# Kernel optimization log

Hardware: AMD Instinct MI355X
Metric: run time of the kernel (lower is better)

The kernel has to match this reference:

```python
import jax, jax.numpy as jnp
import numpy as np

NEG_SLOPE = 0.2  # PyG GATConv default leaky_relu slope


def gat_conv(x, src, dst, W, a_src, a_dst, b, num_nodes):
    """One PyG-style GATConv layer (concat over heads).
    x: [N, F_in]; src/dst: [E] (message flows src -> dst);
    W: [F_in, H*C]; a_src/a_dst: [H, C]; b: [H*C].
    """
    H, C = a_src.shape
    h = (x @ W).reshape(num_nodes, H, C)              # [N, H, C]
    alpha_src = jnp.sum(h * a_src, axis=-1)           # [N, H]
    alpha_dst = jnp.sum(h * a_dst, axis=-1)           # [N, H]
    e = jax.nn.leaky_relu(alpha_src[src] + alpha_dst[dst], NEG_SLOPE)  # [E, H]
    # segment softmax over incoming edges of each destination node
    m = jax.ops.segment_max(e, dst, num_segments=num_nodes)            # [N, H]
    ex = jnp.exp(e - m[dst])
    s = jax.ops.segment_sum(ex, dst, num_segments=num_nodes)           # [N, H]
    alpha = ex / (s[dst] + 1e-16)                                      # [E, H]
    msg = h[src] * alpha[:, :, None]                                   # [E, H, C]
    out = jax.ops.segment_sum(msg, dst, num_segments=num_nodes)        # [N, H, C]
    return out.reshape(num_nodes, H * C) + b


def setup_inputs() -> dict:
    key = jax.random.key(0)
    ks = jax.random.split(key, 12)
    N, E, F_in, C, H = 50000, 800000, 256, 64, 8
    x = jax.random.normal(ks[0], (N, F_in), dtype=jnp.float32)
    edge_index = jax.random.randint(ks[1], (2, E), 0, N, dtype=jnp.int64)
    glorot = lambda k, shape: jax.random.normal(k, shape, jnp.float32) * np.sqrt(2.0 / (shape[0] + shape[-1]))
    return {
        "x": x,
        "edge_index": edge_index,
        "W1": glorot(ks[2], (F_in, H * C)),
        "att_src1": glorot(ks[3], (H, C)),
        "att_dst1": glorot(ks[4], (H, C)),
        "b1": jnp.zeros((H * C,), jnp.float32),
        "W2": glorot(ks[5], (H * C, 1 * C)),
        "att_src2": glorot(ks[6], (1, C)),
        "att_dst2": glorot(ks[7], (1, C)),
        "b2": jnp.zeros((C,), jnp.float32),
    }


def reference(x, edge_index, W1, att_src1, att_dst1, b1, W2, att_src2, att_dst2, b2):
    N = x.shape[0]
    # add self-loops (PyG GATConv default add_self_loops=True)
    loops = jnp.arange(N, dtype=edge_index.dtype)
    src = jnp.concatenate([edge_index[0], loops])
    dst = jnp.concatenate([edge_index[1], loops])
    h = gat_conv(x, src, dst, W1, att_src1, att_dst1, b1, N)   # [N, 512]
    h = jax.nn.relu(h)                                         # dropout p=0 -> identity
    out = gat_conv(h, src, dst, W2, att_src2, att_dst2, b2, N) # [N, 64]
    return out
```

## Files before the change

### kernel.cpp

```cpp
#include <hip/hip_runtime.h>
#include <hip/hip_bf16.h>
#include <math.h>
#include <type_traits>

#define NEG_SLOPE 0.2f
#define CAP 64

typedef float f32x4 __attribute__((ext_vector_type(4)));
typedef short s16x8 __attribute__((ext_vector_type(8)));
typedef short s16x4 __attribute__((ext_vector_type(4)));

__device__ __forceinline__ float bf2f(ushort s) {
    union { unsigned u; float f; } cv; cv.u = ((unsigned)s) << 16;
    return cv.f;
}
__device__ __forceinline__ ushort f2bf(float f) {
    __hip_bfloat16 b = __float2bfloat16(f);
    union { __hip_bfloat16 b; ushort u; } cv; cv.b = b;
    return cv.u;
}

__device__ __forceinline__ int edge_val(const int* e, long long i, int is64) {
    return is64 ? e[(size_t)(2 * i)] : e[(size_t)i];
}

__global__ void prep_all(const int* __restrict__ e, int* __restrict__ flag,
                         int* __restrict__ counts, int* __restrict__ csr, int N,
                         const float* __restrict__ W1, ushort* __restrict__ W1t, int K1, int N1,
                         const float* __restrict__ W2, ushort* __restrict__ W2t, int K2, int N2) {
    int b = blockIdx.x, tid = threadIdx.x;
    int nbN = (N + 255) >> 8;
    int nbW1 = (K1 * N1 + 255) >> 8;
    if (b < nbN) {
        int i = b * 256 + tid;
        if (i < N) {
            counts[i] = 1;
            csr[(size_t)i * CAP] = i;
        }
    } else if (b == nbN) {
        if (tid < 64) {
            int v = e[2 * tid + 1];
            unsigned long long bl = __ballot(v != 0);
            if (tid == 0) *flag = (bl == 0ull) ? 1 : 0;
        }
    } else if (b < nbN + 1 + nbW1) {
        int idx = (b - nbN - 1) * 256 + tid;
        if (idx < K1 * N1) {
            int k = idx & (K1 - 1), n = idx / K1;
            W1t[(size_t)n * K1 + k] = f2bf(W1[(size_t)k * N1 + n]);
        }
    } else {
        int idx = (b - nbN - 1 - nbW1) * 256 + tid;
        if (idx < K2 * N2) {
            int k = idx & (K2 - 1), n = idx / K2;
            W2t[(size_t)n * K2 + k] = f2bf(W2[(size_t)k * N2 + n]);
        }
    }
}

__global__ void scatter_edges(const int* __restrict__ ebuf, int E,
                              int* __restrict__ counts, int* __restrict__ csr,
                              const int* __restrict__ flag) {
    int i = blockIdx.x * blockDim.x + threadIdx.x;
    if (i >= E) return;
    int is64 = *flag;
    int s = edge_val(ebuf, i, is64);
    int d = edge_val(ebuf, (long long)E + i, is64);
    int pos = atomicAdd(&counts[d], 1);
    if (pos < CAP) csr[(size_t)d * CAP + pos] = s;
}

template <typename AT, typename CT, int BM, int BN, int WR, int WC, int H>
__global__ __launch_bounds__(256) void gemm_mfma(const AT* __restrict__ A,
                                                 const ushort* __restrict__ Bt,
                                                 CT* __restrict__ C,
                                                 const float* __restrict__ att_s,
                                                 const float* __restrict__ att_d,
                                                 float* __restrict__ as_,
                                                 float* __restrict__ ad_,
                                                 int M, int N, int K) {
    constexpr int BK = 64;
    constexpr int MT = BM / WR / 16;
    constexpr int NT = 4;
    static_assert(WR * WC == 4 && BN == WC * 64, "4 waves, 64 cols each");
    __shared__ __align__(16) ushort As[BM][BK + 8];
    __shared__ __align__(16) ushort Bs[BN][BK + 8];

    int tid = threadIdx.x;
    int wid = tid >> 6, lane = tid & 63;
    int wr = wid / WC, wc = wid % WC;
    int bm = blockIdx.y * BM, bn = blockIdx.x * BN;
    int l15 = lane & 15, l4 = lane >> 4;

    f32x4 acc[MT][NT] = {};

    for (int k0 = 0; k0 < K; k0 += BK) {
        if constexpr (std::is_same_v<AT, float>) {
#pragma unroll
            for (int p = 0; p < BM * BK / 1024; ++p) {
                int idx = p * 256 + tid;
                int r = idx >> 4;
                int kc = (idx & 15) << 2;
                float4 v = make_float4(0.f, 0.f, 0.f, 0.f);
                if (bm + r < M) v = *(const float4*)&A[(size_t)(bm + r) * K + k0 + kc];
                ushort* dst = &As[r][kc];
                dst[0] = f2bf(v.x); dst[1] = f2bf(v.y);
                dst[2] = f2bf(v.z); dst[3] = f2bf(v.w);
            }
        } else {
#pragma unroll
            for (int p = 0; p < BM * BK / 2048; ++p) {
                int idx = p * 256 + tid;
                int r = idx >> 3;
                int kc = (idx & 7) << 3;
                s16x8 v = {};
                if (bm + r < M) v = *(const s16x8*)&A[(size_t)(bm + r) * K + k0 + kc];
                *(s16x8*)&As[r][kc] = v;
            }
        }
#pragma unroll
        for (int p = 0; p < BN * BK / 2048; ++p) {
            int idx = p * 256 + tid;
            int n = idx >> 3;
            int kc = (idx & 7) << 3;
            s16x8 v = *(const s16x8*)&Bt[(size_t)(bn + n) * K + k0 + kc];
            *(s16x8*)&Bs[n][kc] = v;
        }
        __syncthreads();
#pragma unroll
        for (int kk = 0; kk < BK; kk += 32) {
            s16x8 af[MT], bf[NT];
            int kb = kk + (l4 << 3);
#pragma unroll
            for (int mt = 0; mt < MT; ++mt)
                af[mt] = *(const s16x8*)&As[wr * (BM / WR) + mt * 16 + l15][kb];
#pragma unroll
            for (int nt = 0; nt < NT; ++nt)
                bf[nt] = *(const s16x8*)&Bs[wc * 64 + nt * 16 + l15][kb];
#pragma unroll
            for (int mt = 0; mt < MT; ++mt)
#pragma unroll
                for (int nt = 0; nt < NT; ++nt)
                    acc[mt][nt] = __builtin_amdgcn_mfma_f32_16x16x32_bf16(af[mt], bf[nt], acc[mt][nt], 0, 0, 0);
        }
        __syncthreads();
    }

    int head = (bn >> 6) + wc;
    float asv[NT], adv[NT];
#pragma unroll
    for (int nt = 0; nt < NT; ++nt) {
        asv[nt] = att_s[head * 64 + nt * 16 + l15];
        adv[nt] = att_d[head * 64 + nt * 16 + l15];
    }
#pragma unroll
    for (int mt = 0; mt < MT; ++mt) {
#pragma unroll
        for (int j = 0; j < 4; ++j) {
            int r = bm + wr * (BM / WR) + mt * 16 + (l4 << 2) + j;
            float ps = 0.f, pd = 0.f;
#pragma unroll
            for (int nt = 0; nt < NT; ++nt) {
                float v = acc[mt][nt][j];
                ps += v * asv[nt];
                pd += v * adv[nt];
            }
#pragma unroll
            for (int off = 1; off < 16; off <<= 1) {
                ps += __shfl_xor(ps, off);
                pd += __shfl_xor(pd, off);
            }
            if (r < M) {
                if (l15 == 0) {
                    as_[(size_t)r * H + head] = ps;
                    ad_[(size_t)r * H + head] = pd;
                }
#pragma unroll
                for (int nt = 0; nt < NT; ++nt) {
                    size_t ci = (size_t)r * N + bn + wc * 64 + nt * 16 + l15;
                    if constexpr (std::is_same_v<CT, float>) C[ci] = acc[mt][nt][j];
                    else C[ci] = f2bf(acc[mt][nt][j]);
                }
            }
        }
    }
}

__global__ __launch_bounds__(256) void gat_fused_l1(
        const ushort* __restrict__ h, const float* __restrict__ as_,
        const float* __restrict__ ad_, const int* __restrict__ counts,
        const int* __restrict__ csr, const float* __restrict__ bias,
        ushort* __restrict__ out1, int N) {
    int n = (blockIdx.x * 256 + threadIdx.x) >> 6;
    if (n >= N) return;
    int l = threadIdx.x & 63;
    size_t base = (size_t)n * CAP;
    int deg = counts[n]; deg = deg > CAP ? CAP : deg;

    int hh = l & 7, e0 = l >> 3;
    float adw = ad_[n * 8 + hh];
    float m = -1e30f, s = 0.f;
    for (int k = e0; k < deg; k += 8) {
        int src = csr[base + k];
        float e = as_[src * 8 + hh] + adw;
        e = e > 0.f ? e : NEG_SLOPE * e;
        float mn = fmaxf(m, e);
        s = s * __expf(m - mn) + __expf(e - mn);
        m = mn;
    }
#pragma unroll
    for (int off = 8; off < 64; off <<= 1) {
        float mo = __shfl_xor(m, off), so = __shfl_xor(s, off);
        float mn = fmaxf(m, mo);
        s = s * __expf(m - mn) + so * __expf(mo - mn);
        m = mn;
    }
    float inv = 1.f / (s + 1e-16f);
    int hd = l >> 3;
    float mh   = __shfl(m, hd);
    float invh = __shfl(inv, hd);
    float adh  = __shfl(adw, hd);

    float acc[8] = {};
    int k = 0;
    for (; k + 4 <= deg; k += 4) {
        int s0 = csr[base + k],     s1 = csr[base + k + 1];
        int s2 = csr[base + k + 2], s3 = csr[base + k + 3];
        s16x8 v0 = *(const s16x8*)&h[((size_t)s0 << 9) + (l << 3)];
        s16x8 v1 = *(const s16x8*)&h[((size_t)s1 << 9) + (l << 3)];
        s16x8 v2 = *(const s16x8*)&h[((size_t)s2 << 9) + (l << 3)];
        s16x8 v3 = *(const s16x8*)&h[((size_t)s3 << 9) + (l << 3)];
        float e0v = as_[s0 * 8 + hd] + adh;
        float e1v = as_[s1 * 8 + hd] + adh;
        float e2v = as_[s2 * 8 + hd] + adh;
        float e3v = as_[s3 * 8 + hd] + adh;
        e0v = e0v > 0.f ? e0v : NEG_SLOPE * e0v;
        e1v = e1v > 0.f ? e1v : NEG_SLOPE * e1v;
        e2v = e2v > 0.f ? e2v : NEG_SLOPE * e2v;
        e3v = e3v > 0.f ? e3v : NEG_SLOPE * e3v;
        float a0 = __expf(e0v - mh);
        float a1 = __expf(e1v - mh);
        float a2 = __expf(e2v - mh);
        float a3 = __expf(e3v - mh);
#pragma unroll
        for (int j = 0; j < 8; ++j)
            acc[j] += a0 * bf2f((ushort)v0[j]) + a1 * bf2f((ushort)v1[j])
                    + a2 * bf2f((ushort)v2[j]) + a3 * bf2f((ushort)v3[j]);
    }
    for (; k < deg; ++k) {
        int s0 = csr[base + k];
        s16x8 v0 = *(const s16x8*)&h[((size_t)s0 << 9) + (l << 3)];
        float e0v = as_[s0 * 8 + hd] + adh;
        e0v = e0v > 0.f ? e0v : NEG_SLOPE * e0v;
        float a0 = __expf(e0v - mh);
#pragma unroll
        for (int j = 0; j < 8; ++j) acc[j] += a0 * bf2f((ushort)v0[j]);
    }
    float4 b0 = *(const float4*)&bias[l * 8];
    float4 b1 = *(const float4*)&bias[l * 8 + 4];
    s16x8 w;
    w[0] = f2bf(fmaxf(acc[0] * invh + b0.x, 0.f));
    w[1] = f2bf(fmaxf(acc[1] * invh + b0.y, 0.f));
    w[2] = f2bf(fmaxf(acc[2] * invh + b0.z, 0.f));
    w[3] = f2bf(fmaxf(acc[3] * invh + b0.w, 0.f));
    w[4] = f2bf(fmaxf(acc[4] * invh + b1.x, 0.f));
    w[5] = f2bf(fmaxf(acc[5] * invh + b1.y, 0.f));
    w[6] = f2bf(fmaxf(acc[6] * invh + b1.z, 0.f));
    w[7] = f2bf(fmaxf(acc[7] * invh + b1.w, 0.f));
    *(s16x8*)&out1[((size_t)n << 9) + (l << 3)] = w;
}

__global__ __launch_bounds__(256) void gat_fused_l2(
        const ushort* __restrict__ h, const float* __restrict__ as_,
        const float* __restrict__ ad_, const int* __restrict__ counts,
        const int* __restrict__ csr, const float* __restrict__ bias,
        float* __restrict__ out, int N) {
    int n = (blockIdx.x * 256 + threadIdx.x) >> 6;
    if (n >= N) return;
    int l = threadIdx.x & 63;
    size_t base = (size_t)n * CAP;
    int deg = counts[n]; deg = deg > CAP ? CAP : deg;
    float adv = ad_[n];

    float m = -1e30f, s = 0.f;
    for (int k = l; k < deg; k += 64) {
        float e = as_[csr[base + k]] + adv;
        e = e > 0.f ? e : NEG_SLOPE * e;
        float mn = fmaxf(m, e);
        s = s * __expf(m - mn) + __expf(e - mn);
        m = mn;
    }
#pragma unroll
    for (int off = 1; off < 64; off <<= 1) {
        float mo = __shfl_xor(m, off), so = __shfl_xor(s, off);
        float mn = fmaxf(m, mo);
        s = s * __expf(m - mn) + so * __expf(mo - mn);
        m = mn;
    }
    float inv = 1.f / (s + 1e-16f);

    int q = l >> 4, c4 = l & 15;
    float a0 = 0.f, a1 = 0.f, a2 = 0.f, a3 = 0.f;
    int k = q;
    for (; k + 12 < deg; k += 16) {
        int sA = csr[base + k],     sB = csr[base + k + 4];
        int sC = csr[base + k + 8], sD = csr[base + k + 12];
        s16x4 vA = *(const s16x4*)&h[((size_t)sA << 6) + (c4 << 2)];
        s16x4 vB = *(const s16x4*)&h[((size_t)sB << 6) + (c4 << 2)];
        s16x4 vC = *(const s16x4*)&h[((size_t)sC << 6) + (c4 << 2)];
        s16x4 vD = *(const s16x4*)&h[((size_t)sD << 6) + (c4 << 2)];
        float eA = as_[sA] + adv, eB = as_[sB] + adv;
        float eC = as_[sC] + adv, eD = as_[sD] + adv;
        eA = eA > 0.f ? eA : NEG_SLOPE * eA;
        eB = eB > 0.f ? eB : NEG_SLOPE * eB;
        eC = eC > 0.f ? eC : NEG_SLOPE * eC;
        eD = eD > 0.f ? eD : NEG_SLOPE * eD;
        float aA = __expf(eA - m), aB = __expf(eB - m);
        float aC = __expf(eC - m), aD = __expf(eD - m);
        a0 += aA * bf2f((ushort)vA[0]) + aB * bf2f((ushort)vB[0])
            + aC * bf2f((ushort)vC[0]) + aD * bf2f((ushort)vD[0]);
        a1 += aA * bf2f((ushort)vA[1]) + aB * bf2f((ushort)vB[1])
            + aC * bf2f((ushort)vC[1]) + aD * bf2f((ushort)vD[1]);
        a2 += aA * bf2f((ushort)vA[2]) + aB * bf2f((ushort)vB[2])
            + aC * bf2f((ushort)vC[2]) + aD * bf2f((ushort)vD[2]);
        a3 += aA * bf2f((ushort)vA[3]) + aB * bf2f((ushort)vB[3])
            + aC * bf2f((ushort)vC[3]) + aD * bf2f((ushort)vD[3]);
    }
    for (; k < deg; k += 4) {
        int sA = csr[base + k];
        s16x4 vA = *(const s16x4*)&h[((size_t)sA << 6) + (c4 << 2)];
        float eA = as_[sA] + adv;
        eA = eA > 0.f ? eA : NEG_SLOPE * eA;
        float aA = __expf(eA - m);
        a0 += aA * bf2f((ushort)vA[0]);
        a1 += aA * bf2f((ushort)vA[1]);
        a2 += aA * bf2f((ushort)vA[2]);
        a3 += aA * bf2f((ushort)vA[3]);
    }
    a0 += __shfl_xor(a0, 16); a0 += __shfl_xor(a0, 32);
    a1 += __shfl_xor(a1, 16); a1 += __shfl_xor(a1, 32);
    a2 += __shfl_xor(a2, 16); a2 += __shfl_xor(a2, 32);
    a3 += __shfl_xor(a3, 16); a3 += __shfl_xor(a3, 32);
    if (q == 0) {
        float4 bv = *(const float4*)&bias[c4 << 2];
        float4 r;
        r.x = a0 * inv + bv.x; r.y = a1 * inv + bv.y;
        r.z = a2 * inv + bv.z; r.w = a3 * inv + bv.w;
        *(float4*)&out[((size_t)n << 6) + (c4 << 2)] = r;
    }
}

extern "C" void kernel_launch(void* const* d_in, const int* in_sizes, int n_in,
                              void* d_out, int out_size, void* d_ws, size_t ws_size,
                              hipStream_t stream) {
    const float* x    = (const float*)d_in[0];
    const int*   ebuf = (const int*)d_in[1];
    const float* W1   = (const float*)d_in[2];
    const float* aS1  = (const float*)d_in[3];
    const float* aD1  = (const float*)d_in[4];
    const float* b1   = (const float*)d_in[5];
    const float* W2   = (const float*)d_in[6];
    const float* aS2  = (const float*)d_in[7];
    const float* aD2  = (const float*)d_in[8];
    const float* b2   = (const float*)d_in[9];
    float* out = (float*)d_out;

    const int F_in = 256, H1 = 8, HC1 = 512, C2 = 64;
    int N = in_sizes[0] / F_in;
    int E = in_sizes[1] / 2;

    char* ws = (char*)d_ws;
    size_t off = 0;
    auto alloc = [&](size_t bytes) -> void* {
        void* p = ws + off;
        off = (off + bytes + 255) & ~(size_t)255;
        return p;
    };
    ushort* h1b    = (ushort*)alloc((size_t)N * HC1 * 2);
    ushort* out1b  = (ushort*)alloc((size_t)N * HC1 * 2);
    float* as1     = (float*)alloc((size_t)N * H1 * 4);
    float* ad1     = (float*)alloc((size_t)N * H1 * 4);
    float* as2     = (float*)alloc((size_t)N * 4);
    float* ad2     = (float*)alloc((size_t)N * 4);
    int*   counts  = (int*)alloc((size_t)N * 4);
    int*   csr     = (int*)alloc((size_t)N * CAP * 4);
    int*   flag    = (int*)alloc(64);
    ushort* W1t    = (ushort*)alloc((size_t)F_in * HC1 * 2);
    ushort* W2t    = (ushort*)alloc((size_t)HC1 * C2 * 2);
    ushort* h2b    = h1b;

    int nbN = (N + 255) >> 8;
    int nbW1 = (F_in * HC1 + 255) >> 8;
    int nbW2 = (HC1 * C2 + 255) >> 8;

    prep_all<<<nbN + 1 + nbW1 + nbW2, 256, 0, stream>>>(
        ebuf, flag, counts, csr, N, W1, W1t, F_in, HC1, W2, W2t, HC1, C2);
    scatter_edges<<<(E + 255) / 256, 256, 0, stream>>>(ebuf, E, counts, csr, flag);

    {
        dim3 g(HC1 / 128, (N + 127) / 128);
        gemm_mfma<float, ushort, 128, 128, 2, 2, 8><<<g, 256, 0, stream>>>(
            x, W1t, h1b, aS1, aD1, as1, ad1, N, HC1, F_in);
    }
    gat_fused_l1<<<(N + 3) / 4, 256, 0, stream>>>(h1b, as1, ad1, counts, csr, b1, out1b, N);

    {
        dim3 g(1, (N + 63) / 64);
        gemm_mfma<ushort, ushort, 64, 64, 4, 1, 1><<<g, 256, 0, stream>>>(
            out1b, W2t, h2b, aS2, aD2, as2, ad2, N, C2, HC1);
    }
    gat_fused_l2<<<(N + 3) / 4, 256, 0, stream>>>(h2b, as2, ad2, counts, csr, b2, out, N);
}
```

Measured before the change: 306.3 us.

## Merge edge scatter into first GEMM launch with wider 512-thread tiles

The separate scatter_edges kernel is folded into the layer-1 GEMM launch. Leading blocks do the atomic CSR fill, and the remaining blocks run the GEMM, so the two independent pieces of work overlap in one launch. The GEMM core becomes a device function generic over wave count, and layer 1 now uses 128x256 tiles with 8 waves (512 threads). The larger tiles roughly double shared memory per block and raise register pressure, which may lower occupancy.

```diff
diff --git a/kernel.cpp b/kernel.cpp
--- a/kernel.cpp
+++ b/kernel.cpp
@@ -58,38 +58,29 @@
     }
 }
 
-__global__ void scatter_edges(const int* __restrict__ ebuf, int E,
-                              int* __restrict__ counts, int* __restrict__ csr,
-                              const int* __restrict__ flag) {
-    int i = blockIdx.x * blockDim.x + threadIdx.x;
-    if (i >= E) return;
-    int is64 = *flag;
-    int s = edge_val(ebuf, i, is64);
-    int d = edge_val(ebuf, (long long)E + i, is64);
-    int pos = atomicAdd(&counts[d], 1);
-    if (pos < CAP) csr[(size_t)d * CAP + pos] = s;
-}
-
 template <typename AT, typename CT, int BM, int BN, int WR, int WC, int H>
-__global__ __launch_bounds__(256) void gemm_mfma(const AT* __restrict__ A,
-                                                 const ushort* __restrict__ Bt,
-                                                 CT* __restrict__ C,
-                                                 const float* __restrict__ att_s,
-                                                 const float* __restrict__ att_d,
-                                                 float* __restrict__ as_,
-                                                 float* __restrict__ ad_,
-                                                 int M, int N, int K) {
+__device__ __forceinline__ void gemm_core(int bx, int by,
+                                          const AT* __restrict__ A,
+                                          const ushort* __restrict__ Bt,
+                                          CT* __restrict__ C,
+                                          const float* __restrict__ att_s,
+                                          const float* __restrict__ att_d,
+                                          float* __restrict__ as_,
+                                          float* __restrict__ ad_,
+                                          int M, int N, int K) {
     constexpr int BK = 64;
+    constexpr int WAVES = WR * WC;
+    constexpr int THREADS = WAVES * 64;
     constexpr int MT = BM / WR / 16;
     constexpr int NT = 4;
-    static_assert(WR * WC == 4 && BN == WC * 64, "4 waves, 64 cols each");
+    static_assert(BN == WC * 64, "each wave-col owns one 64-col head");
     __shared__ __align__(16) ushort As[BM][BK + 8];
     __shared__ __align__(16) ushort Bs[BN][BK + 8];
 
     int tid = threadIdx.x;
     int wid = tid >> 6, lane = tid & 63;
     int wr = wid / WC, wc = wid % WC;
-    int bm = blockIdx.y * BM, bn = blockIdx.x * BN;
+    int bm = by * BM, bn = bx * BN;
     int l15 = lane & 15, l4 = lane >> 4;
 
     f32x4 acc[MT][NT] = {};
@@ -97,8 +88,8 @@
     for (int k0 = 0; k0 < K; k0 += BK) {
         if constexpr (std::is_same_v<AT, float>) {
 #pragma unroll
-            for (int p = 0; p < BM * BK / 1024; ++p) {
-                int idx = p * 256 + tid;
+            for (int p = 0; p < BM * BK / (4 * THREADS); ++p) {
+                int idx = p * THREADS + tid;
                 int r = idx >> 4;
                 int kc = (idx & 15) << 2;
                 float4 v = make_float4(0.f, 0.f, 0.f, 0.f);
@@ -109,8 +100,8 @@
             }
         } else {
 #pragma unroll
-            for (int p = 0; p < BM * BK / 2048; ++p) {
-                int idx = p * 256 + tid;
+            for (int p = 0; p < BM * BK / (8 * THREADS); ++p) {
+                int idx = p * THREADS + tid;
                 int r = idx >> 3;
                 int kc = (idx & 7) << 3;
                 s16x8 v = {};
@@ -119,8 +110,8 @@
             }
         }
 #pragma unroll
-        for (int p = 0; p < BN * BK / 2048; ++p) {
-            int idx = p * 256 + tid;
+        for (int p = 0; p < BN * BK / (8 * THREADS); ++p) {
+            int idx = p * THREADS + tid;
             int n = idx >> 3;
             int kc = (idx & 7) << 3;
             s16x8 v = *(const s16x8*)&Bt[(size_t)(bn + n) * K + k0 + kc];
@@ -184,6 +175,37 @@
             }
         }
     }
+}
+
+__global__ __launch_bounds__(512) void gemm1_scatter(
+        const int* __restrict__ ebuf, int E, int* __restrict__ counts,
+        int* __restrict__ csr, const int* __restrict__ flag, int nScatter,
+        const float* __restrict__ A, const ushort* __restrict__ Bt,
+        ushort* __restrict__ C, const float* __restrict__ att_s,
+        const float* __restrict__ att_d, float* __restrict__ as_,
+        float* __restrict__ ad_, int M, int N, int K) {
+    if ((int)blockIdx.x < nScatter) {
+        int i = blockIdx.x * 512 + threadIdx.x;
+        if (i >= E) return;
+        int is64 = *flag;
+        int s = edge_val(ebuf, i, is64);
+        int d = edge_val(ebuf, (long long)E + i, is64);
+        int pos = atomicAdd(&counts[d], 1);
+        if (pos < CAP) csr[(size_t)d * CAP + pos] = s;
+        return;
+    }
+    int g = blockIdx.x - nScatter;
+    gemm_core<float, ushort, 128, 256, 2, 4, 8>(g & 1, g >> 1, A, Bt, C,
+                                                att_s, att_d, as_, ad_, M, N, K);
+}
+
+template <typename AT, typename CT, int BM, int BN, int WR, int WC, int H>
+__global__ __launch_bounds__(WR * WC * 64) void gemm_mfma(
+        const AT* __restrict__ A, const ushort* __restrict__ Bt, CT* __restrict__ C,
+        const float* __restrict__ att_s, const float* __restrict__ att_d,
+        float* __restrict__ as_, float* __restrict__ ad_, int M, int N, int K) {
+    gemm_core<AT, CT, BM, BN, WR, WC, H>(blockIdx.x, blockIdx.y, A, Bt, C,
+                                         att_s, att_d, as_, ad_, M, N, K);
 }
 
 __global__ __launch_bounds__(256) void gat_fused_l1(
@@ -395,13 +417,15 @@
 
     prep_all<<<nbN + 1 + nbW1 + nbW2, 256, 0, stream>>>(
         ebuf, flag, counts, csr, N, W1, W1t, F_in, HC1, W2, W2t, HC1, C2);
-    scatter_edges<<<(E + 255) / 256, 256, 0, stream>>>(ebuf, E, counts, csr, flag);
 
     {
-        dim3 g(HC1 / 128, (N + 127) / 128);
-        gemm_mfma<float, ushort, 128, 128, 2, 2, 8><<<g, 256, 0, stream>>>(
+        int nScatter = (E + 511) / 512;
+        int nGemm = 2 * ((N + 127) / 128);
+        gemm1_scatter<<<nScatter + nGemm, 512, 0, stream>>>(
+            ebuf, E, counts, csr, flag, nScatter,
             x, W1t, h1b, aS1, aD1, as1, ad1, N, HC1, F_in);
     }
+
     gat_fused_l1<<<(N + 3) / 4, 256, 0, stream>>>(h1b, as1, ad1, counts, csr, b1, out1b, N);
 
     {
```

New measurement: 303.9 us. About the same (-0.8%).
